# Kernel tuning notes

Measured on AMD Instinct MI355X. Metric: run time of the kernel, lower is better.

Reference implementation:

```python
import jax, jax.numpy as jnp
import numpy as np
from jax import lax

B, T, I, H, O = 64, 512, 64, 1024, 64

def setup_inputs() -> dict:
    key = jax.random.key(0)
    ks = jax.random.split(key, 8)
    s_ih = 1.0 / np.sqrt(H)
    return {
        "x": jax.random.normal(ks[0], (B, T, I), dtype=jnp.float32),
        "hidden": jnp.zeros((1, B, H), dtype=jnp.float32),
        "W_ih": jax.random.uniform(ks[1], (H, I), jnp.float32, -s_ih, s_ih),
        "W_hh": jax.random.uniform(ks[2], (H, H), jnp.float32, -s_ih, s_ih),
        "b_ih": jax.random.uniform(ks[3], (H,), jnp.float32, -s_ih, s_ih),
        "b_hh": jax.random.uniform(ks[4], (H,), jnp.float32, -s_ih, s_ih),
        "W_out": jax.random.uniform(ks[5], (O, H), jnp.float32, -s_ih, s_ih),
        "b_out": jax.random.uniform(ks[6], (O,), jnp.float32, -s_ih, s_ih),
    }

def reference(x, hidden, W_ih, W_hh, b_ih, b_hh, W_out, b_out):
    # Precompute input projection for all timesteps in one GEMM: [B,T,H]
    xw = jnp.einsum('bti,hi->bth', x, W_ih) + b_ih + b_hh
    h0 = hidden[0]  # [B,H]

    def step(h, xw_t):
        h_new = jax.nn.relu(xw_t + h @ W_hh.T)  # relu(W_ih x + b_ih + W_hh h + b_hh)
        return h_new, h_new

    h_last, hs = lax.scan(step, h0, xw.transpose(1, 0, 2))  # hs: [T,B,H]
    hidden_list = hs.transpose(1, 0, 2)  # [B,T,H]
    output_list = jnp.einsum('bth,oh->bto', hidden_list, W_out) + b_out  # [B,T,O]
    return hidden_list, output_list, h_last[None]
```

## Files before the change

### kernel.cpp

```cpp
#include <hip/hip_runtime.h>
#include <hip/hip_bf16.h>

#define B_  64
#define T_  512
#define I_  64
#define H_  1024
#define O_  64

typedef __bf16 bf16x8 __attribute__((ext_vector_type(8)));
typedef unsigned short u16x8 __attribute__((ext_vector_type(8)));
typedef float f32x4 __attribute__((ext_vector_type(4)));
typedef unsigned int u32;
typedef unsigned long long u64;

static __device__ __forceinline__ f32x4 mfma16(bf16x8 a, bf16x8 b, f32x4 c) {
  return __builtin_amdgcn_mfma_f32_16x16x32_bf16(a, b, c, 0, 0, 0);
}

static __device__ __forceinline__ bf16x8 cvt8(const float* __restrict__ p) {
  f32x4 v0 = *(const f32x4*)p;
  f32x4 v1 = *(const f32x4*)(p + 4);
  bf16x8 r;
  r[0] = (__bf16)v0[0]; r[1] = (__bf16)v0[1];
  r[2] = (__bf16)v0[2]; r[3] = (__bf16)v0[3];
  r[4] = (__bf16)v1[0]; r[5] = (__bf16)v1[1];
  r[6] = (__bf16)v1[2]; r[7] = (__bf16)v1[3];
  return r;
}

static __device__ __forceinline__ bool valid_u32(u32 w, u32 gen) {
  return ((u32)((w & 0xFFFFu) - 1u) <= 0x7F80u) && ((w >> 31) == gen);
}
static __device__ __forceinline__ bool valid_u64(u64 w, u32 gen) {
  return valid_u32((u32)w, gen) && valid_u32((u32)(w >> 32), gen);
}
static __device__ __forceinline__ u64 decode_u64(u64 w) {
  return (w - 0x0001000100010001ULL) & 0x7FFF7FFF7FFF7FFFULL;
}

__global__ void __launch_bounds__(512) k_rec(
    const float* __restrict__ x, const float* __restrict__ h0,
    const float* __restrict__ Wih, const float* __restrict__ Whh,
    const float* __restrict__ bih, const float* __restrict__ bhh,
    float* __restrict__ hidden_out, unsigned short* __restrict__ buf)
{
  __shared__ unsigned short hlds[16 * 1024];

  const int bid = blockIdx.x;
  const int g = bid >> 3;
  const int j = bid & 7;
  const int tid = threadIdx.x;
  const int wv = tid >> 6;
  const int l  = tid & 63;
  const int l4 = l >> 4, lm = l & 15;

  const int nrow = j * 128 + wv * 16 + lm;
  const int ab   = g * 16 + lm;

  u16x8 bw[32];
  #pragma unroll
  for (int kk = 0; kk < 32; ++kk)
    bw[kk] = __builtin_bit_cast(u16x8, cvt8(Whh + nrow * H_ + kk * 32 + l4 * 8));
  u16x8 bwi0 = __builtin_bit_cast(u16x8, cvt8(Wih + nrow * I_ + 0  + l4 * 8));
  u16x8 bwi1 = __builtin_bit_cast(u16x8, cvt8(Wih + nrow * I_ + 32 + l4 * 8));
  const float bias = bih[nrow] + bhh[nrow];

  const int lrow = tid >> 5;
  const int q    = tid & 31;

  char* ldsb = (char*)hlds;
  const int sw_w = (lrow & 7) << 4;

  for (int s = 1; s <= T_; ++s) {
    const float* xr = x + ((size_t)ab * T_ + (s - 1)) * I_ + l4 * 8;
    f32x4 xv0 = *(const f32x4*)xr;
    f32x4 xv1 = *(const f32x4*)(xr + 4);
    f32x4 y0  = *(const f32x4*)(xr + 32);
    f32x4 y1  = *(const f32x4*)(xr + 36);

    if (s == 1) {
      const float* hp = h0 + (size_t)(g * 16 + lrow) * H_ + q * 8;
      #pragma unroll
      for (int c = 0; c < 4; ++c) {
        bf16x8 hb = cvt8(hp + c * 256);
        int byteoff = (lrow * 2048 + q * 16 + c * 512) ^ sw_w;
        *(u16x8*)(ldsb + byteoff) = __builtin_bit_cast(u16x8, hb);
      }
    } else {
      const u32 gen = (u32)(((s - 1) >> 1) & 1);
      const u64* hp = (const u64*)(buf + (size_t)((s - 1) & 1) * (B_ * H_)) +
                      (size_t)(g * 16 + lrow) * 256 + q * 2;
      u32 vmask = 0;
      do {
        u32 prev = vmask;
        #pragma unroll
        for (int c = 0; c < 4; ++c) {
          if (vmask & (1u << c)) continue;
          u64 lo = __hip_atomic_load(hp + c * 64 + 0, __ATOMIC_RELAXED,
                                     __HIP_MEMORY_SCOPE_AGENT);
          u64 hi = __hip_atomic_load(hp + c * 64 + 1, __ATOMIC_RELAXED,
                                     __HIP_MEMORY_SCOPE_AGENT);
          if (valid_u64(lo, gen) && valid_u64(hi, gen)) {
            vmask |= 1u << c;
            int byteoff = (lrow * 2048 + q * 16 + c * 512) ^ sw_w;
            *(u64*)(ldsb + byteoff) = decode_u64(lo);
            *(u64*)(ldsb + byteoff + 8) = decode_u64(hi);
          }
        }
        if (vmask == prev) __builtin_amdgcn_s_sleep(1);
      } while (vmask != 0xFu);
    }
    __syncthreads();

    f32x4 accx = {0.f, 0.f, 0.f, 0.f};
    {
      bf16x8 xa0, xa1;
      xa0[0]=(__bf16)xv0[0]; xa0[1]=(__bf16)xv0[1]; xa0[2]=(__bf16)xv0[2]; xa0[3]=(__bf16)xv0[3];
      xa0[4]=(__bf16)xv1[0]; xa0[5]=(__bf16)xv1[1]; xa0[6]=(__bf16)xv1[2]; xa0[7]=(__bf16)xv1[3];
      xa1[0]=(__bf16)y0[0]; xa1[1]=(__bf16)y0[1]; xa1[2]=(__bf16)y0[2]; xa1[3]=(__bf16)y0[3];
      xa1[4]=(__bf16)y1[0]; xa1[5]=(__bf16)y1[1]; xa1[6]=(__bf16)y1[2]; xa1[7]=(__bf16)y1[3];
      accx = mfma16(xa0, __builtin_bit_cast(bf16x8, bwi0), accx);
      accx = mfma16(xa1, __builtin_bit_cast(bf16x8, bwi1), accx);
    }

    f32x4 a0 = {0,0,0,0}, a1 = {0,0,0,0}, a2 = {0,0,0,0}, a3 = {0,0,0,0};
    #pragma unroll
    for (int kk = 0; kk < 32; kk += 4) {
      int base = lm * 2048 + l4 * 16;
      int sw = (lm & 7) << 4;
      u16x8 h0v = *(const u16x8*)(ldsb + ((base + (kk + 0) * 64) ^ sw));
      u16x8 h1v = *(const u16x8*)(ldsb + ((base + (kk + 1) * 64) ^ sw));
      u16x8 h2v = *(const u16x8*)(ldsb + ((base + (kk + 2) * 64) ^ sw));
      u16x8 h3v = *(const u16x8*)(ldsb + ((base + (kk + 3) * 64) ^ sw));
      a0 = mfma16(__builtin_bit_cast(bf16x8, h0v), __builtin_bit_cast(bf16x8, bw[kk + 0]), a0);
      a1 = mfma16(__builtin_bit_cast(bf16x8, h1v), __builtin_bit_cast(bf16x8, bw[kk + 1]), a1);
      a2 = mfma16(__builtin_bit_cast(bf16x8, h2v), __builtin_bit_cast(bf16x8, bw[kk + 2]), a2);
      a3 = mfma16(__builtin_bit_cast(bf16x8, h3v), __builtin_bit_cast(bf16x8, bw[kk + 3]), a3);
    }
    f32x4 acc = (a0 + a1) + (a2 + a3) + accx;

    unsigned short* bp = buf + (size_t)(s & 1) * (B_ * H_);
    const u32 genw = (u32)((s >> 1) & 1);
    float vv[4];
    u32 enc[4];
    #pragma unroll
    for (int r = 0; r < 4; ++r) {
      float v = acc[r] + bias;
      v = v > 0.f ? v : 0.f;
      vv[r] = v;
      enc[r] = (u32)__builtin_bit_cast(unsigned short, (__bf16)v) + 1u;
    }
    #pragma unroll
    for (int r = 0; r < 4; ++r) {
      u32 partner = (u32)__shfl_xor((int)enc[r], 1, 64);
      if ((lm & 1) == 0) {
        u32 two = enc[r] | (partner << 16) | (genw << 31);
        int b = g * 16 + l4 * 4 + r;
        __hip_atomic_store((u32*)(bp + (size_t)b * H_ + nrow), two,
                           __ATOMIC_RELAXED, __HIP_MEMORY_SCOPE_AGENT);
      }
    }
    #pragma unroll
    for (int r = 0; r < 4; ++r) {
      int b = g * 16 + l4 * 4 + r;
      hidden_out[((size_t)b * T_ + (s - 1)) * H_ + nrow] = vv[r];
    }

    __syncthreads();
  }
}

__global__ void __launch_bounds__(256) k_out(
    const float* __restrict__ hidden, const float* __restrict__ Wout,
    const float* __restrict__ bout, float* __restrict__ out,
    float* __restrict__ hlast)
{
  int idx = blockIdx.x * 256 + threadIdx.x;
  for (int i = idx; i < B_ * H_; i += gridDim.x * 256)
    hlast[i] = hidden[(size_t)(i >> 10) * (T_ * H_) + (size_t)(T_ - 1) * H_ + (i & (H_ - 1))];

  const int wv = threadIdx.x >> 6;
  const int l  = threadIdx.x & 63;
  const int l4 = l >> 4, lm = l & 15;
  const int rt = blockIdx.x * 4 + wv;
  const int rowA = rt * 16 + lm;

  f32x4 acc0 = {0,0,0,0}, acc1 = {0,0,0,0}, acc2 = {0,0,0,0}, acc3 = {0,0,0,0};
  float bo0 = bout[0 * 16 + lm], bo1 = bout[1 * 16 + lm];
  float bo2 = bout[2 * 16 + lm], bo3 = bout[3 * 16 + lm];

  #pragma unroll
  for (int kk = 0; kk < 32; ++kk) {
    bf16x8 a = cvt8(hidden + (size_t)rowA * H_ + kk * 32 + l4 * 8);
    acc0 = mfma16(a, cvt8(Wout + (size_t)(0 * 16 + lm) * H_ + kk * 32 + l4 * 8), acc0);
    acc1 = mfma16(a, cvt8(Wout + (size_t)(1 * 16 + lm) * H_ + kk * 32 + l4 * 8), acc1);
    acc2 = mfma16(a, cvt8(Wout + (size_t)(2 * 16 + lm) * H_ + kk * 32 + l4 * 8), acc2);
    acc3 = mfma16(a, cvt8(Wout + (size_t)(3 * 16 + lm) * H_ + kk * 32 + l4 * 8), acc3);
  }

  #pragma unroll
  for (int r = 0; r < 4; ++r) {
    int row = rt * 16 + l4 * 4 + r;
    out[(size_t)row * O_ + 0 * 16 + lm] = acc0[r] + bo0;
    out[(size_t)row * O_ + 1 * 16 + lm] = acc1[r] + bo1;
    out[(size_t)row * O_ + 2 * 16 + lm] = acc2[r] + bo2;
    out[(size_t)row * O_ + 3 * 16 + lm] = acc3[r] + bo3;
  }
}

extern "C" void kernel_launch(void* const* d_in, const int* in_sizes, int n_in,
                              void* d_out, int out_size, void* d_ws, size_t ws_size,
                              hipStream_t stream) {
  const float* x    = (const float*)d_in[0];
  const float* h0   = (const float*)d_in[1];
  const float* Wih  = (const float*)d_in[2];
  const float* Whh  = (const float*)d_in[3];
  const float* bih  = (const float*)d_in[4];
  const float* bhh  = (const float*)d_in[5];
  const float* Wout = (const float*)d_in[6];
  const float* bout = (const float*)d_in[7];

  float* out = (float*)d_out;
  float* hidden_out  = out;
  float* output_list = out + (size_t)B_ * T_ * H_;
  float* hlast       = output_list + (size_t)B_ * T_ * O_;

  unsigned short* buf = (unsigned short*)output_list;

  k_rec<<<32, 512, 0, stream>>>(x, h0, Wih, Whh, bih, bhh, hidden_out, buf);
  k_out<<<512, 256, 0, stream>>>(hidden_out, Wout, bout, output_list, hlast);
}
```

Before: 2.495 ms.

## Double-buffer LDS hidden state, write own slice locally, drop trailing barrier

The hidden-state LDS buffer is now double-buffered, which makes the end-of-step __syncthreads unnecessary, so only one barrier per timestep remains. Each block writes its own freshly computed hidden slice straight into the next step's LDS buffer and skips polling global memory for it. The poll loop switches to finer 8-byte chunks with a per-lane rotated start order to spread the load traffic. The intent is less barrier and global-polling latency on the serial recurrence critical path, at the cost of double the LDS footprint and more fine-grained atomic loads.

```diff
diff --git a/kernel.cpp b/kernel.cpp
--- a/kernel.cpp
+++ b/kernel.cpp
@@ -28,6 +28,12 @@
   return r;
 }
 
+static __device__ __forceinline__ u32 pack_bf16x2(float a, float b) {
+  unsigned short lo = __builtin_bit_cast(unsigned short, (__bf16)a);
+  unsigned short hi = __builtin_bit_cast(unsigned short, (__bf16)b);
+  return (u32)lo | ((u32)hi << 16);
+}
+
 static __device__ __forceinline__ bool valid_u32(u32 w, u32 gen) {
   return ((u32)((w & 0xFFFFu) - 1u) <= 0x7F80u) && ((w >> 31) == gen);
 }
@@ -44,7 +50,7 @@
     const float* __restrict__ bih, const float* __restrict__ bhh,
     float* __restrict__ hidden_out, unsigned short* __restrict__ buf)
 {
-  __shared__ unsigned short hlds[16 * 1024];
+  __shared__ unsigned short hlds[2 * 16 * 1024];
 
   const int bid = blockIdx.x;
   const int g = bid >> 3;
@@ -68,10 +74,12 @@
   const int lrow = tid >> 5;
   const int q    = tid & 31;
 
-  char* ldsb = (char*)hlds;
   const int sw_w = (lrow & 7) << 4;
+  const u32 own  = 1u << j;
 
   for (int s = 1; s <= T_; ++s) {
+    char* ldsc = (char*)hlds + (size_t)(s & 1) * 32768;
+
     const float* xr = x + ((size_t)ab * T_ + (s - 1)) * I_ + l4 * 8;
     f32x4 xv0 = *(const f32x4*)xr;
     f32x4 xv1 = *(const f32x4*)(xr + 4);
@@ -79,38 +87,36 @@
     f32x4 y1  = *(const f32x4*)(xr + 36);
 
     if (s == 1) {
-      const float* hp = h0 + (size_t)(g * 16 + lrow) * H_ + q * 8;
+      const float* hp = h0 + (size_t)(g * 16 + lrow) * H_ + q * 4;
       #pragma unroll
-      for (int c = 0; c < 4; ++c) {
-        bf16x8 hb = cvt8(hp + c * 256);
-        int byteoff = (lrow * 2048 + q * 16 + c * 512) ^ sw_w;
-        *(u16x8*)(ldsb + byteoff) = __builtin_bit_cast(u16x8, hb);
+      for (int c = 0; c < 8; ++c) {
+        f32x4 v = *(const f32x4*)(hp + c * 128);
+        u64 w = (u64)pack_bf16x2(v[0], v[1]) |
+                ((u64)pack_bf16x2(v[2], v[3]) << 32);
+        *(u64*)(ldsc + ((lrow * 2048 + c * 256 + q * 8) ^ sw_w)) = w;
       }
     } else {
       const u32 gen = (u32)(((s - 1) >> 1) & 1);
-      const u64* hp = (const u64*)(buf + (size_t)((s - 1) & 1) * (B_ * H_)) +
-                      (size_t)(g * 16 + lrow) * 256 + q * 2;
-      u32 vmask = 0;
+      const u64* basep = (const u64*)(buf + (size_t)((s - 1) & 1) * (B_ * H_)) +
+                         (size_t)(g * 16 + lrow) * 256 + q;
+      u32 vmask = own;
       do {
         u32 prev = vmask;
         #pragma unroll
-        for (int c = 0; c < 4; ++c) {
+        for (int cc = 0; cc < 8; ++cc) {
+          int c = (cc + (q & 7)) & 7;
           if (vmask & (1u << c)) continue;
-          u64 lo = __hip_atomic_load(hp + c * 64 + 0, __ATOMIC_RELAXED,
-                                     __HIP_MEMORY_SCOPE_AGENT);
-          u64 hi = __hip_atomic_load(hp + c * 64 + 1, __ATOMIC_RELAXED,
-                                     __HIP_MEMORY_SCOPE_AGENT);
-          if (valid_u64(lo, gen) && valid_u64(hi, gen)) {
+          u64 w = __hip_atomic_load(basep + c * 32, __ATOMIC_RELAXED,
+                                    __HIP_MEMORY_SCOPE_AGENT);
+          if (valid_u64(w, gen)) {
             vmask |= 1u << c;
-            int byteoff = (lrow * 2048 + q * 16 + c * 512) ^ sw_w;
-            *(u64*)(ldsb + byteoff) = decode_u64(lo);
-            *(u64*)(ldsb + byteoff + 8) = decode_u64(hi);
+            *(u64*)(ldsc + ((lrow * 2048 + c * 256 + q * 8) ^ sw_w)) =
+                decode_u64(w);
           }
         }
         if (vmask == prev) __builtin_amdgcn_s_sleep(1);
-      } while (vmask != 0xFu);
-    }
-    __syncthreads();
+      } while (vmask != 0xFFu);
+    }
 
     f32x4 accx = {0.f, 0.f, 0.f, 0.f};
     {
@@ -122,16 +128,17 @@
       accx = mfma16(xa0, __builtin_bit_cast(bf16x8, bwi0), accx);
       accx = mfma16(xa1, __builtin_bit_cast(bf16x8, bwi1), accx);
     }
+    __syncthreads();
 
     f32x4 a0 = {0,0,0,0}, a1 = {0,0,0,0}, a2 = {0,0,0,0}, a3 = {0,0,0,0};
     #pragma unroll
     for (int kk = 0; kk < 32; kk += 4) {
       int base = lm * 2048 + l4 * 16;
       int sw = (lm & 7) << 4;
-      u16x8 h0v = *(const u16x8*)(ldsb + ((base + (kk + 0) * 64) ^ sw));
-      u16x8 h1v = *(const u16x8*)(ldsb + ((base + (kk + 1) * 64) ^ sw));
-      u16x8 h2v = *(const u16x8*)(ldsb + ((base + (kk + 2) * 64) ^ sw));
-      u16x8 h3v = *(const u16x8*)(ldsb + ((base + (kk + 3) * 64) ^ sw));
+      u16x8 h0v = *(const u16x8*)(ldsc + ((base + (kk + 0) * 64) ^ sw));
+      u16x8 h1v = *(const u16x8*)(ldsc + ((base + (kk + 1) * 64) ^ sw));
+      u16x8 h2v = *(const u16x8*)(ldsc + ((base + (kk + 2) * 64) ^ sw));
+      u16x8 h3v = *(const u16x8*)(ldsc + ((base + (kk + 3) * 64) ^ sw));
       a0 = mfma16(__builtin_bit_cast(bf16x8, h0v), __builtin_bit_cast(bf16x8, bw[kk + 0]), a0);
       a1 = mfma16(__builtin_bit_cast(bf16x8, h1v), __builtin_bit_cast(bf16x8, bw[kk + 1]), a1);
       a2 = mfma16(__builtin_bit_cast(bf16x8, h2v), __builtin_bit_cast(bf16x8, bw[kk + 2]), a2);
@@ -139,34 +146,36 @@
     }
     f32x4 acc = (a0 + a1) + (a2 + a3) + accx;
 
-    unsigned short* bp = buf + (size_t)(s & 1) * (B_ * H_);
+    char* ldsn = (char*)hlds + (size_t)((s + 1) & 1) * 32768;
+    u32* bp = (u32*)(buf + (size_t)(s & 1) * (B_ * H_));
     const u32 genw = (u32)((s >> 1) & 1);
     float vv[4];
     u32 enc[4];
     #pragma unroll
     for (int r = 0; r < 4; ++r) {
+      int b2 = l4 * 4 + r;
       float v = acc[r] + bias;
       v = v > 0.f ? v : 0.f;
       vv[r] = v;
       enc[r] = (u32)__builtin_bit_cast(unsigned short, (__bf16)v) + 1u;
+      int off = (b2 * 2048 + nrow * 2) ^ ((b2 & 7) << 4);
+      *(unsigned short*)(ldsn + off) = __builtin_bit_cast(unsigned short, (__bf16)v);
     }
     #pragma unroll
     for (int r = 0; r < 4; ++r) {
       u32 partner = (u32)__shfl_xor((int)enc[r], 1, 64);
       if ((lm & 1) == 0) {
+        int b2 = l4 * 4 + r;
         u32 two = enc[r] | (partner << 16) | (genw << 31);
-        int b = g * 16 + l4 * 4 + r;
-        __hip_atomic_store((u32*)(bp + (size_t)b * H_ + nrow), two,
+        __hip_atomic_store(bp + (((size_t)(g * 16 + b2) * H_ + nrow) >> 1), two,
                            __ATOMIC_RELAXED, __HIP_MEMORY_SCOPE_AGENT);
       }
     }
     #pragma unroll
     for (int r = 0; r < 4; ++r) {
-      int b = g * 16 + l4 * 4 + r;
-      hidden_out[((size_t)b * T_ + (s - 1)) * H_ + nrow] = vv[r];
-    }
-
-    __syncthreads();
+      int b2 = l4 * 4 + r;
+      hidden_out[((size_t)(g * 16 + b2) * T_ + (s - 1)) * H_ + nrow] = vv[r];
+    }
   }
 }
 
```

New measurement: 3.585 ms. 1.44x slower.
